# Kernel tuning notes

Measured on AMD Instinct MI355X. Metric: run time of the kernel, lower is better.

Reference implementation:

```python
import jax, jax.numpy as jnp
import numpy as np

N_NODES = 50000
IN_CH = 128
HID = 128
OUT_CH = 40
N_LAYERS = 3
N_EDGES = 600000


def setup_inputs() -> dict:
    key = jax.random.key(0)
    ks = jax.random.split(key, 4 + 5 * N_LAYERS)
    x = jax.random.normal(ks[0], (N_NODES, IN_CH), dtype=jnp.float32)
    edge_attr = jax.random.normal(ks[1], (N_EDGES, 4), dtype=jnp.float32)
    edge_index = jax.random.randint(ks[2], (2, N_EDGES), 0, N_NODES, dtype=jnp.int64)
    # Per-layer MLP params ([in->hid->hid]); in==hid so stack as [L, d, d].
    def glorot(k, fan_in, fan_out):
        s = jnp.sqrt(2.0 / (fan_in + fan_out)).astype(jnp.float32)
        return jax.random.normal(k, (fan_in, fan_out), dtype=jnp.float32) * s
    W1 = jnp.stack([glorot(ks[3 + i], IN_CH if i == 0 else HID, HID) for i in range(N_LAYERS)])
    b1 = jnp.zeros((N_LAYERS, HID), dtype=jnp.float32)
    W2 = jnp.stack([glorot(ks[3 + N_LAYERS + i], HID, HID) for i in range(N_LAYERS)])
    b2 = jnp.zeros((N_LAYERS, HID), dtype=jnp.float32)
    Wc = glorot(ks[3 + 2 * N_LAYERS], HID, OUT_CH)
    bc = jnp.zeros((OUT_CH,), dtype=jnp.float32)
    return {"x": x, "edge_attr": edge_attr, "edge_index": edge_index,
            "W1": W1, "b1": b1, "W2": W2, "b2": b2, "Wc": Wc, "bc": bc}


def reference(x, edge_attr, edge_index, W1, b1, W2, b2, Wc, bc):
    # GIN node classifier, eval mode (dropout = identity, BN = identity).
    src, dst = edge_index[0], edge_index[1]
    h = x
    for i in range(N_LAYERS):
        # GINConv (eps=0): aggregate sum of neighbor features via scatter-add.
        msgs = h[src]                                   # [E, d] gather
        aggr = jax.ops.segment_sum(msgs, dst, num_segments=N_NODES)  # [N, d]
        z = h + aggr                                    # (1+eps)*x + sum
        z = jax.nn.relu(z @ W1[i] + b1[i])              # MLP hidden
        z = z @ W2[i] + b2[i]                           # MLP out
        h = jax.nn.relu(z)                              # F.relu(conv(...))
    return h @ Wc + bc                                  # [N, OUT_CH]
```

## Files before the change

### kernel.cpp

```cpp
#include <hip/hip_runtime.h>

#define N_NODES 50000
#define IN_CH 128
#define HID 128
#define OUT_CH 40
#define N_LAYERS 3
#define N_EDGES 600000
#define DSTRIDE 64

typedef __attribute__((ext_vector_type(8))) short short8;
typedef __attribute__((ext_vector_type(4))) float floatx4;

static __device__ __forceinline__ unsigned short f32_to_bf16(float f) {
  unsigned u = __float_as_uint(f);
  unsigned r = 0x7FFFu + ((u >> 16) & 1u);
  return (unsigned short)((u + r) >> 16);
}
static __device__ __forceinline__ float bf16_to_f32(unsigned short h) {
  return __uint_as_float(((unsigned)h) << 16);
}

#define CONV_BLOCKS 6250
#define W_BLOCKS 408
#define DEG_BLOCKS 49
#define COL_MAX (N_NODES * DSTRIDE)
#define COLF_BLOCKS 3125

__global__ __launch_bounds__(256) void prep_all_kernel(
    const float* __restrict__ x, const float* __restrict__ W1,
    const float* __restrict__ W2, const float* __restrict__ Wc,
    unsigned short* __restrict__ xb, unsigned short* __restrict__ WT,
    unsigned short* __restrict__ WcT, unsigned short* __restrict__ hb1,
    int* __restrict__ deg, int* __restrict__ col) {
  const int b = blockIdx.x;
  const int t = threadIdx.x;
  if (b < CONV_BLOCKS) {
    int i = (b * 256 + t) * 4;
    if (i < N_NODES * 128) {
      float4 v = *(const float4*)(x + i);
      ushort4 o;
      o.x = f32_to_bf16(v.x); o.y = f32_to_bf16(v.y);
      o.z = f32_to_bf16(v.z); o.w = f32_to_bf16(v.w);
      *(ushort4*)(xb + i) = o;
    }
  } else if (b < CONV_BLOCKS + W_BLOCKS) {
    int o = (b - CONV_BLOCKS) * 256 + t;
    if (o < 6 * 16384) {
      int mat = o >> 14;
      int r = o & 16383;
      int n = r >> 7;
      int k = r & 127;
      const float* W = (mat < 3) ? (W1 + (size_t)mat * 16384)
                                 : (W2 + (size_t)(mat - 3) * 16384);
      WT[(size_t)mat * 16384 + (size_t)n * 128 + k] =
          f32_to_bf16(W[(size_t)k * 128 + n]);
    } else if (o < 6 * 16384 + 48 * 128) {
      int r = o - 6 * 16384;
      int n = r >> 7;
      int k = r & 127;
      float v = (n < OUT_CH) ? Wc[(size_t)k * OUT_CH + n] : 0.0f;
      WcT[(size_t)n * 128 + k] = f32_to_bf16(v);
    }
  } else if (b < CONV_BLOCKS + W_BLOCKS + DEG_BLOCKS) {
    int i = ((b - CONV_BLOCKS - W_BLOCKS) * 256 + t) * 4;
    if (i + 3 < N_NODES) {
      *(int4*)(deg + i) = make_int4(0, 0, 0, 0);
    } else {
      for (int k = 0; k < 4; ++k)
        if (i + k < N_NODES) deg[i + k] = 0;
    }
  } else if (b < CONV_BLOCKS + W_BLOCKS + DEG_BLOCKS + COLF_BLOCKS) {
    int i = ((b - CONV_BLOCKS - W_BLOCKS - DEG_BLOCKS) * 256 + t) * 4;
    *(int4*)(col + i) = make_int4(N_NODES, N_NODES, N_NODES, N_NODES);
  } else {
    if (t < 128) xb[(size_t)N_NODES * 128 + t] = 0;
    else hb1[(size_t)N_NODES * 128 + (t - 128)] = 0;
  }
}

__global__ __launch_bounds__(256) void csr_kernel(
    const int* __restrict__ ei, int* __restrict__ deg, int* __restrict__ col) {
  int e = blockIdx.x * 256 + threadIdx.x;
  if (e >= N_EDGES) return;
  int s = ei[e];
  int d = ei[N_EDGES + e];
  int pos = atomicAdd(&deg[d], 1);
  col[(size_t)d * DSTRIDE + pos] = s;
}

__global__ __launch_bounds__(256) void aggregate_kernel(
    const unsigned short* __restrict__ h, const int* __restrict__ deg,
    const int* __restrict__ col, unsigned short* __restrict__ z) {
  int n = __builtin_amdgcn_readfirstlane(blockIdx.x * 4 + (threadIdx.x >> 6));
  int q = threadIdx.x & 63;
  const size_t co = (size_t)q * 2;
  ushort2 sv = *(const ushort2*)(h + (size_t)n * 128 + co);
  float ax[8], ay[8];
#pragma unroll
  for (int k = 0; k < 8; ++k) { ax[k] = 0.f; ay[k] = 0.f; }
  ax[0] = bf16_to_f32(sv.x);
  ay[0] = bf16_to_f32(sv.y);
  int dg = __builtin_amdgcn_readfirstlane(deg[n]);
  int cnt = (dg + 15) & ~15;
  const int* cp = col + (size_t)n * DSTRIDE;
  for (int i = 0; i < cnt; i += 16) {
    int ss[16];
#pragma unroll
    for (int k = 0; k < 16; ++k)
      ss[k] = __builtin_amdgcn_readfirstlane(cp[i + k]);
    ushort2 vv[16];
#pragma unroll
    for (int k = 0; k < 16; ++k)
      vv[k] = *(const ushort2*)(h + (size_t)ss[k] * 128 + co);
#pragma unroll
    for (int k = 0; k < 16; ++k) {
      ax[k & 7] += bf16_to_f32(vv[k].x);
      ay[k & 7] += bf16_to_f32(vv[k].y);
    }
  }
  float s0 = (ax[0] + ax[1]) + (ax[2] + ax[3]) + (ax[4] + ax[5]) + (ax[6] + ax[7]);
  float s1 = (ay[0] + ay[1]) + (ay[2] + ay[3]) + (ay[4] + ay[5]) + (ay[6] + ay[7]);
  ushort2 o;
  o.x = f32_to_bf16(s0);
  o.y = f32_to_bf16(s1);
  *(ushort2*)(z + (size_t)n * 128 + co) = o;
}

template <bool LAST>
__global__ __launch_bounds__(256) void layer_pair_kernel(
    const unsigned short* __restrict__ A, const unsigned short* __restrict__ WT1,
    const float* __restrict__ b1, const unsigned short* __restrict__ WT2,
    const float* __restrict__ b2, unsigned short* __restrict__ Z,
    const unsigned short* __restrict__ WcT, const float* __restrict__ bc,
    float* __restrict__ out, int M) {
  __shared__ __align__(16) unsigned short Wl[128][136];
  __shared__ __align__(16) unsigned short T[64][136];
  const int tid = threadIdx.x;
  const int w = tid >> 6;
  const int lane = tid & 63;
  const int qg = lane >> 4;
  const int ln = lane & 15;
  const int row0 = blockIdx.x * 64;
  const int rbase = w * 16;
  const int r0 = row0 + rbase + ln;
  const short8 zero8 = {0, 0, 0, 0, 0, 0, 0, 0};

#pragma unroll
  for (int j = 0; j < 8; ++j) {
    int slot = tid + j * 256;
    int row = slot >> 4;
    int kb = slot & 15;
    *(short8*)&Wl[row][kb * 8] = *(const short8*)(WT1 + (size_t)row * 128 + kb * 8);
  }
  __syncthreads();

  floatx4 acc[8];
#pragma unroll
  for (int ct = 0; ct < 8; ++ct) acc[ct] = (floatx4){0.f, 0.f, 0.f, 0.f};
#pragma unroll
  for (int ks = 0; ks < 4; ++ks) {
    const int koff = ks * 32 + qg * 8;
    short8 a = (r0 < M) ? *(const short8*)(A + (size_t)r0 * 128 + koff) : zero8;
#pragma unroll
    for (int ct = 0; ct < 8; ++ct) {
      short8 b = *(const short8*)&Wl[ct * 16 + ln][koff];
      acc[ct] = __builtin_amdgcn_mfma_f32_16x16x32_bf16(a, b, acc[ct], 0, 0, 0);
    }
  }
#pragma unroll
  for (int ct = 0; ct < 8; ++ct) {
    float bv = b1[ct * 16 + ln];
#pragma unroll
    for (int r = 0; r < 4; ++r) {
      float v = fmaxf(acc[ct][r] + bv, 0.0f);
      T[rbase + qg * 4 + r][ct * 16 + ln] = f32_to_bf16(v);
    }
  }

  __syncthreads();
#pragma unroll
  for (int j = 0; j < 8; ++j) {
    int slot = tid + j * 256;
    int row = slot >> 4;
    int kb = slot & 15;
    *(short8*)&Wl[row][kb * 8] = *(const short8*)(WT2 + (size_t)row * 128 + kb * 8);
  }
  __syncthreads();

  floatx4 acc2[8];
#pragma unroll
  for (int ct = 0; ct < 8; ++ct) acc2[ct] = (floatx4){0.f, 0.f, 0.f, 0.f};
#pragma unroll
  for (int ks = 0; ks < 4; ++ks) {
    const int koff = ks * 32 + qg * 8;
    short8 a = *(const short8*)&T[rbase + ln][koff];
#pragma unroll
    for (int ct = 0; ct < 8; ++ct) {
      short8 b = *(const short8*)&Wl[ct * 16 + ln][koff];
      acc2[ct] = __builtin_amdgcn_mfma_f32_16x16x32_bf16(a, b, acc2[ct], 0, 0, 0);
    }
  }
#pragma unroll
  for (int ct = 0; ct < 8; ++ct) {
    float bv = b2[ct * 16 + ln];
#pragma unroll
    for (int r = 0; r < 4; ++r) {
      float v = fmaxf(acc2[ct][r] + bv, 0.0f);
      T[rbase + qg * 4 + r][ct * 16 + ln] = f32_to_bf16(v);
    }
  }

  if (LAST) {
    floatx4 acc3[3];
#pragma unroll
    for (int ct = 0; ct < 3; ++ct) acc3[ct] = (floatx4){0.f, 0.f, 0.f, 0.f};
#pragma unroll
    for (int ks = 0; ks < 4; ++ks) {
      const int koff = ks * 32 + qg * 8;
      short8 a = *(const short8*)&T[rbase + ln][koff];
#pragma unroll
      for (int ct = 0; ct < 3; ++ct) {
        short8 b = *(const short8*)(WcT + (size_t)(ct * 16 + ln) * 128 + koff);
        acc3[ct] = __builtin_amdgcn_mfma_f32_16x16x32_bf16(a, b, acc3[ct], 0, 0, 0);
      }
    }
#pragma unroll
    for (int ct = 0; ct < 3; ++ct) {
      int colg = ct * 16 + ln;
      if (colg < OUT_CH) {
        float bv = bc[colg];
#pragma unroll
        for (int r = 0; r < 4; ++r) {
          int row = row0 + rbase + qg * 4 + r;
          if (row < M) out[(size_t)row * OUT_CH + colg] = acc3[ct][r] + bv;
        }
      }
    }
  } else {
    __syncthreads();
#pragma unroll
    for (int j = 0; j < 4; ++j) {
      int slot = tid + j * 256;
      int row = slot >> 4;
      int kb = slot & 15;
      if (row0 + row < M) {
        short8 v = *(const short8*)&T[row][kb * 8];
        *(short8*)(Z + (size_t)(row0 + row) * 128 + kb * 8) = v;
      }
    }
  }
}

extern "C" void kernel_launch(void* const* d_in, const int* in_sizes, int n_in,
                              void* d_out, int out_size, void* d_ws,
                              size_t ws_size, hipStream_t stream) {
  const float* x = (const float*)d_in[0];
  const int* ei = (const int*)d_in[2];
  const float* W1 = (const float*)d_in[3];
  const float* b1 = (const float*)d_in[4];
  const float* W2 = (const float*)d_in[5];
  const float* b2 = (const float*)d_in[6];
  const float* Wc = (const float*)d_in[7];
  const float* bc = (const float*)d_in[8];
  float* out = (float*)d_out;

  const size_t NF = (size_t)(N_NODES + 1) * 128;
  unsigned short* hb0 = (unsigned short*)d_ws;
  unsigned short* hb1 = hb0 + NF;
  unsigned short* xbf = hb1 + NF;
  unsigned short* WT = xbf + NF;
  unsigned short* WcT = WT + 6 * 16384;
  int* deg = (int*)(WcT + 48 * 128);
  int* col = deg + N_NODES;

  const dim3 blk(256);
  const int edge_grid = (N_EDGES + 255) / 256;
  const int aggr_grid = N_NODES / 4;
  const int pair_grid = (N_NODES + 63) / 64;

  prep_all_kernel<<<CONV_BLOCKS + W_BLOCKS + DEG_BLOCKS + COLF_BLOCKS + 1, blk,
                    0, stream>>>(x, W1, W2, Wc, xbf, WT, WcT, hb1, deg, col);

  csr_kernel<<<edge_grid, blk, 0, stream>>>(ei, deg, col);

  const unsigned short* h = xbf;
  for (int l = 0; l < N_LAYERS; ++l) {
    aggregate_kernel<<<aggr_grid, blk, 0, stream>>>(h, deg, col, hb0);
    if (l < N_LAYERS - 1) {
      layer_pair_kernel<false><<<pair_grid, blk, 0, stream>>>(
          hb0, WT + (size_t)l * 16384, b1 + (size_t)l * 128,
          WT + (size_t)(3 + l) * 16384, b2 + (size_t)l * 128, hb1,
          nullptr, nullptr, nullptr, N_NODES);
      h = hb1;
    } else {
      layer_pair_kernel<true><<<pair_grid, blk, 0, stream>>>(
          hb0, WT + (size_t)l * 16384, b1 + (size_t)l * 128,
          WT + (size_t)(3 + l) * 16384, b2 + (size_t)l * 128, nullptr,
          WcT, bc, out, N_NODES);
    }
  }
}
```

Baseline: 251.2 us.

## Store CSR indices as uint16 and gather two neighbors per wave

Adjacency column indices drop from int32 to uint16, which is valid because the node count and the padding sentinel both fit in 16 bits. This halves the bytes written when filling and building the adjacency list and halves the bytes read in aggregation. The aggregate kernel now splits each wave into two halves that gather different neighbors using 8-byte bf16x4 loads, then combines the halves with a cross-lane shuffle. This is meant to cut instruction count and index-load traffic per neighbor, at the cost of a shuffle reduction and idle lanes on the final store.

```diff
diff --git a/kernel.cpp b/kernel.cpp
--- a/kernel.cpp
+++ b/kernel.cpp
@@ -24,14 +24,14 @@
 #define W_BLOCKS 408
 #define DEG_BLOCKS 49
 #define COL_MAX (N_NODES * DSTRIDE)
-#define COLF_BLOCKS 3125
+#define COLF_BLOCKS 1563
 
 __global__ __launch_bounds__(256) void prep_all_kernel(
     const float* __restrict__ x, const float* __restrict__ W1,
     const float* __restrict__ W2, const float* __restrict__ Wc,
     unsigned short* __restrict__ xb, unsigned short* __restrict__ WT,
     unsigned short* __restrict__ WcT, unsigned short* __restrict__ hb1,
-    int* __restrict__ deg, int* __restrict__ col) {
+    int* __restrict__ deg, unsigned short* __restrict__ col) {
   const int b = blockIdx.x;
   const int t = threadIdx.x;
   if (b < CONV_BLOCKS) {
@@ -70,8 +70,12 @@
         if (i + k < N_NODES) deg[i + k] = 0;
     }
   } else if (b < CONV_BLOCKS + W_BLOCKS + DEG_BLOCKS + COLF_BLOCKS) {
-    int i = ((b - CONV_BLOCKS - W_BLOCKS - DEG_BLOCKS) * 256 + t) * 4;
-    *(int4*)(col + i) = make_int4(N_NODES, N_NODES, N_NODES, N_NODES);
+    int i = ((b - CONV_BLOCKS - W_BLOCKS - DEG_BLOCKS) * 256 + t) * 8;
+    if (i + 7 < COL_MAX) {
+      const short p = (short)(unsigned short)N_NODES;
+      short8 v = {p, p, p, p, p, p, p, p};
+      *(short8*)(col + i) = v;
+    }
   } else {
     if (t < 128) xb[(size_t)N_NODES * 128 + t] = 0;
     else hb1[(size_t)N_NODES * 128 + (t - 128)] = 0;
@@ -79,51 +83,72 @@
 }
 
 __global__ __launch_bounds__(256) void csr_kernel(
-    const int* __restrict__ ei, int* __restrict__ deg, int* __restrict__ col) {
+    const int* __restrict__ ei, int* __restrict__ deg,
+    unsigned short* __restrict__ col) {
   int e = blockIdx.x * 256 + threadIdx.x;
   if (e >= N_EDGES) return;
   int s = ei[e];
   int d = ei[N_EDGES + e];
   int pos = atomicAdd(&deg[d], 1);
-  col[(size_t)d * DSTRIDE + pos] = s;
+  col[(size_t)d * DSTRIDE + pos] = (unsigned short)s;
 }
 
 __global__ __launch_bounds__(256) void aggregate_kernel(
     const unsigned short* __restrict__ h, const int* __restrict__ deg,
-    const int* __restrict__ col, unsigned short* __restrict__ z) {
+    const unsigned short* __restrict__ col, unsigned short* __restrict__ z) {
   int n = __builtin_amdgcn_readfirstlane(blockIdx.x * 4 + (threadIdx.x >> 6));
   int q = threadIdx.x & 63;
-  const size_t co = (size_t)q * 2;
-  ushort2 sv = *(const ushort2*)(h + (size_t)n * 128 + co);
-  float ax[8], ay[8];
-#pragma unroll
-  for (int k = 0; k < 8; ++k) { ax[k] = 0.f; ay[k] = 0.f; }
-  ax[0] = bf16_to_f32(sv.x);
-  ay[0] = bf16_to_f32(sv.y);
+  const int half = q >> 5;
+  const size_t co = (size_t)(q & 31) * 4;
+  float acc[4][4];
+#pragma unroll
+  for (int k = 0; k < 4; ++k)
+#pragma unroll
+    for (int c = 0; c < 4; ++c) acc[k][c] = 0.f;
+  {
+    ushort4 sv = *(const ushort4*)(h + (size_t)n * 128 + co);
+    if (half == 0) {
+      acc[0][0] = bf16_to_f32(sv.x); acc[0][1] = bf16_to_f32(sv.y);
+      acc[0][2] = bf16_to_f32(sv.z); acc[0][3] = bf16_to_f32(sv.w);
+    }
+  }
   int dg = __builtin_amdgcn_readfirstlane(deg[n]);
   int cnt = (dg + 15) & ~15;
-  const int* cp = col + (size_t)n * DSTRIDE;
+  const unsigned int* cp32 =
+      (const unsigned int*)(col + (size_t)n * DSTRIDE);
   for (int i = 0; i < cnt; i += 16) {
-    int ss[16];
-#pragma unroll
-    for (int k = 0; k < 16; ++k)
-      ss[k] = __builtin_amdgcn_readfirstlane(cp[i + k]);
-    ushort2 vv[16];
-#pragma unroll
-    for (int k = 0; k < 16; ++k)
-      vv[k] = *(const ushort2*)(h + (size_t)ss[k] * 128 + co);
-#pragma unroll
-    for (int k = 0; k < 16; ++k) {
-      ax[k & 7] += bf16_to_f32(vv[k].x);
-      ay[k & 7] += bf16_to_f32(vv[k].y);
-    }
-  }
-  float s0 = (ax[0] + ax[1]) + (ax[2] + ax[3]) + (ax[4] + ax[5]) + (ax[6] + ax[7]);
-  float s1 = (ay[0] + ay[1]) + (ay[2] + ay[3]) + (ay[4] + ay[5]) + (ay[6] + ay[7]);
-  ushort2 o;
-  o.x = f32_to_bf16(s0);
-  o.y = f32_to_bf16(s1);
-  *(ushort2*)(z + (size_t)n * 128 + co) = o;
+    unsigned int pr[8];
+#pragma unroll
+    for (int k = 0; k < 8; ++k)
+      pr[k] = __builtin_amdgcn_readfirstlane(cp32[(i >> 1) + k]);
+    ushort4 vv[8];
+#pragma unroll
+    for (int k = 0; k < 8; ++k) {
+      int s = half ? (int)(pr[k] >> 16) : (int)(pr[k] & 0xffffu);
+      vv[k] = *(const ushort4*)(h + (size_t)s * 128 + co);
+    }
+#pragma unroll
+    for (int k = 0; k < 8; ++k) {
+      acc[k & 3][0] += bf16_to_f32(vv[k].x);
+      acc[k & 3][1] += bf16_to_f32(vv[k].y);
+      acc[k & 3][2] += bf16_to_f32(vv[k].z);
+      acc[k & 3][3] += bf16_to_f32(vv[k].w);
+    }
+  }
+  float s0 = (acc[0][0] + acc[1][0]) + (acc[2][0] + acc[3][0]);
+  float s1 = (acc[0][1] + acc[1][1]) + (acc[2][1] + acc[3][1]);
+  float s2 = (acc[0][2] + acc[1][2]) + (acc[2][2] + acc[3][2]);
+  float s3 = (acc[0][3] + acc[1][3]) + (acc[2][3] + acc[3][3]);
+  s0 += __shfl_xor(s0, 32, 64);
+  s1 += __shfl_xor(s1, 32, 64);
+  s2 += __shfl_xor(s2, 32, 64);
+  s3 += __shfl_xor(s3, 32, 64);
+  if (half == 0) {
+    ushort4 o;
+    o.x = f32_to_bf16(s0); o.y = f32_to_bf16(s1);
+    o.z = f32_to_bf16(s2); o.w = f32_to_bf16(s3);
+    *(ushort4*)(z + (size_t)n * 128 + co) = o;
+  }
 }
 
 template <bool LAST>
@@ -271,7 +296,7 @@
   unsigned short* WT = xbf + NF;
   unsigned short* WcT = WT + 6 * 16384;
   int* deg = (int*)(WcT + 48 * 128);
-  int* col = deg + N_NODES;
+  unsigned short* col = (unsigned short*)(deg + N_NODES);
 
   const dim3 blk(256);
   const int edge_grid = (N_EDGES + 255) / 256;
```

Result: no change. 251.4 us (+0.1%).
